# Optimization experiments

Measured on AMD Instinct MI355X. Metric: run time of the kernel, lower is better.

Reference implementation:

```python
import jax, jax.numpy as jnp
import numpy as np

B, D, K, H, E, Z = 64, 25000, 16, 128, 256, 32


def setup_inputs() -> dict:
    key = jax.random.key(0)
    ks = jax.random.split(key, 10)
    s = 0.02
    return {
        "x": jax.random.normal(ks[0], (B, D), jnp.float32),
        "mask": jax.random.randint(ks[1], (B, D), 0, 2, jnp.int32),
        "feat_emb": jax.random.normal(ks[2], (D, K), jnp.float32),          # feature_embedding [D,K]
        "feat_bias": jnp.zeros((D, 1), jnp.float32),                        # feature_bias [D,1]
        "W1": jax.random.normal(ks[3], (1 + K + 1, H), jnp.float32) * s,    # h_layer linear 1 (in,out)
        "b1": jnp.zeros((H,), jnp.float32),
        "W2": jax.random.normal(ks[4], (H, K), jnp.float32) * s,            # h_layer linear 2
        "b2": jnp.zeros((K,), jnp.float32),
        "We1": jax.random.normal(ks[5], (K, E), jnp.float32) * s,           # encoder_mlp linear 1
        "be1": jnp.zeros((E,), jnp.float32),
        "We2": jax.random.normal(ks[6], (E, 2 * Z), jnp.float32) * s,       # encoder_mlp linear 2
        "be2": jnp.zeros((2 * Z,), jnp.float32),
    }


def reference(x, mask, feat_emb, feat_bias, W1, b1, W2, b2, We1, be1, We2, be2):
    b, d = x.shape
    k = feat_emb.shape[1]
    # Build per-(sample, feature) input rows: [x_bd, F_d(K), bias_d] -> [B, D, 1+K+1]
    h_in = jnp.concatenate(
        [
            x[:, :, None],
            jnp.broadcast_to(feat_emb[None, :, :], (b, d, k)),
            jnp.broadcast_to(feat_bias[None, :, :], (b, d, 1)),
        ],
        axis=-1,
    )
    # Shared small MLP (h_layer), dropout is identity at rate 0.0
    h = jax.nn.relu(h_in @ W1 + b1)          # [B, D, H]
    h = jax.nn.relu(h @ W2 + b2)             # [B, D, K]
    # Masked sum pooling over features
    c = jnp.sum(h * mask.astype(h.dtype)[:, :, None], axis=1)  # [B, K]
    # encoder_mlp
    enc = jax.nn.relu(c @ We1 + be1) @ We2 + be2                # [B, 2Z]
    mu, logvar = jnp.split(enc, 2, axis=-1)
    return mu, logvar
```

## Files before the change

### kernel.cpp

```cpp
#include <hip/hip_runtime.h>
#include <hip/hip_bf16.h>

#define B 64
#define D 25000
#define K 16
#define H 128
#define E 256
#define Z 32
#define DTILE 20
#define NBLK (D / DTILE)
#define NREP 8
#define MSTR 68

#define REP_BYTES (NREP * B * K * 4)
#define HI_OFF    REP_BYTES

typedef __attribute__((ext_vector_type(8))) _Float16 half8;
typedef __attribute__((ext_vector_type(2))) _Float16 hv2;
typedef __attribute__((ext_vector_type(4))) float f32x4;

__global__ __launch_bounds__(256) void prep_kernel(
    const float* __restrict__ W2, float* __restrict__ rep, _Float16* __restrict__ hi)
{
    const int t = threadIdx.x;
    const int bid = blockIdx.x;
    if (bid < NREP) {
        for (int i = t; i < B * K; i += 256) rep[bid * B * K + i] = 0.f;
    } else {
        for (int i = t; i < H * K; i += 256) {
            int j = i & 7, n = (i >> 3) & 15, g = (i >> 7) & 3, s = i >> 9;
            int k = s * 32 + g * 8 + j;
            hi[i] = (_Float16)W2[k * K + n];
        }
    }
}

__global__ __launch_bounds__(256) void partial_main_kernel(
    const float* __restrict__ x, const int* __restrict__ mask,
    const float* __restrict__ feat_emb, const float* __restrict__ feat_bias,
    const float* __restrict__ W1, const float* __restrict__ b1,
    const float* __restrict__ b2, const _Float16* __restrict__ hi,
    float* __restrict__ rep)
{
    __shared__ __align__(16) _Float16 sGh[DTILE * H];
    __shared__ __align__(16) float sMf[DTILE * MSTR];

    const int t    = threadIdx.x;
    const int d0   = blockIdx.x * DTILE;
    const int lane = t & 63;
    const int wv   = t >> 6;
    const int g    = lane >> 4;
    const int n    = lane & 15;

    for (int i = t; i < DTILE * B; i += 256) {
        int bb = i / DTILE, dd = i - bb * DTILE;
        sMf[dd * MSTR + bb] = (float)mask[bb * D + d0 + dd];
    }
    for (int i = t; i < DTILE * H; i += 256) {
        int dd = i >> 7, h = i & (H - 1);
        int d = d0 + dd;
        float acc = fmaf(feat_bias[d], W1[17 * H + h], b1[h]);
        #pragma unroll
        for (int k = 0; k < K; ++k)
            acc = fmaf(feat_emb[d * K + k], W1[(1 + k) * H + h], acc);
        sGh[i] = (_Float16)acc;
    }

    const float* xrow = x + (size_t)(wv * 16 + n) * D + d0;
    hv2 xh[DTILE / 2];
    #pragma unroll
    for (int i = 0; i < DTILE / 4; ++i) {
        float4 xv = *(const float4*)(xrow + 4 * i);
        xh[2 * i]     = (hv2){(_Float16)xv.x, (_Float16)xv.y};
        xh[2 * i + 1] = (hv2){(_Float16)xv.z, (_Float16)xv.w};
    }

    half8 Bf[4];
    #pragma unroll
    for (int s = 0; s < 4; ++s)
        Bf[s] = *(const half8*)(hi + (((s * 4 + g) * 16 + n) << 3));
    hv2 w0h[4][4];
    #pragma unroll
    for (int s = 0; s < 4; ++s) {
        const float4* wp = (const float4*)&W1[s * 32 + g * 8];
        float4 a0 = wp[0], a1 = wp[1];
        w0h[s][0] = (hv2){(_Float16)a0.x, (_Float16)a0.y};
        w0h[s][1] = (hv2){(_Float16)a0.z, (_Float16)a0.w};
        w0h[s][2] = (hv2){(_Float16)a1.x, (_Float16)a1.y};
        w0h[s][3] = (hv2){(_Float16)a1.z, (_Float16)a1.w};
    }
    const float b2n = b2[n];
    const hv2 zeroh = {(_Float16)0.f, (_Float16)0.f};
    __syncthreads();

    f32x4 cacc = {0.f, 0.f, 0.f, 0.f};
    const int moff = wv * 16 + g * 4;
    const _Float16* gb0 = sGh + g * 8;

    #pragma unroll
    for (int i = 0; i < DTILE / 2; ++i) {
        const int dd0 = 2 * i, dd1 = 2 * i + 1;
        const hv2 xa = {xh[i].x, xh[i].x};
        const hv2 xb = {xh[i].y, xh[i].y};
        f32x4 c1a = {b2n, b2n, b2n, b2n};
        f32x4 c1b = {b2n, b2n, b2n, b2n};
        #pragma unroll
        for (int s = 0; s < 4; ++s) {
            union GA { half8 v; hv2 p[4]; };
            GA ga, gb, A0, A1;
            ga.v = *(const half8*)(gb0 + dd0 * H + s * 32);
            gb.v = *(const half8*)(gb0 + dd1 * H + s * 32);
            #pragma unroll
            for (int p = 0; p < 4; ++p) {
                hv2 h0 = __builtin_elementwise_fma(xa, w0h[s][p], ga.p[p]);
                hv2 h1 = __builtin_elementwise_fma(xb, w0h[s][p], gb.p[p]);
                A0.p[p] = __builtin_elementwise_max(h0, zeroh);
                A1.p[p] = __builtin_elementwise_max(h1, zeroh);
            }
            c1a = __builtin_amdgcn_mfma_f32_16x16x32_f16(A0.v, Bf[s], c1a, 0, 0, 0);
            c1b = __builtin_amdgcn_mfma_f32_16x16x32_f16(A1.v, Bf[s], c1b, 0, 0, 0);
        }
        const float4 mv0 = *(const float4*)&sMf[dd0 * MSTR + moff];
        const float4 mv1 = *(const float4*)&sMf[dd1 * MSTR + moff];
        cacc[0] = fmaf(mv0.x, fmaxf(c1a[0], 0.f), fmaf(mv1.x, fmaxf(c1b[0], 0.f), cacc[0]));
        cacc[1] = fmaf(mv0.y, fmaxf(c1a[1], 0.f), fmaf(mv1.y, fmaxf(c1b[1], 0.f), cacc[1]));
        cacc[2] = fmaf(mv0.z, fmaxf(c1a[2], 0.f), fmaf(mv1.z, fmaxf(c1b[2], 0.f), cacc[2]));
        cacc[3] = fmaf(mv0.w, fmaxf(c1a[3], 0.f), fmaf(mv1.w, fmaxf(c1b[3], 0.f), cacc[3]));
    }

    float* crep = rep + (size_t)(blockIdx.x & (NREP - 1)) * (B * K);
    #pragma unroll
    for (int r = 0; r < 4; ++r)
        atomicAdd(&crep[(moff + r) * K + n], cacc[r]);
}

__global__ __launch_bounds__(256) void partial_enc_kernel(
    const float* __restrict__ rep, const float* __restrict__ We1,
    const float* __restrict__ be1, const float* __restrict__ We2,
    const float* __restrict__ be2, float* __restrict__ out)
{
    const int b = blockIdx.x;
    const int t = threadIdx.x;
    __shared__ float sc[K];
    __shared__ float st1[E];
    __shared__ float red[256];

    {
        const int k = t & 15, grp = t >> 4;
        red[t] = (grp < NREP) ? rep[grp * (B * K) + b * K + k] : 0.f;
    }
    __syncthreads();
    if (t < K) {
        float s2 = 0.f;
        #pragma unroll
        for (int q = 0; q < 16; ++q) s2 += red[q * 16 + t];
        sc[t] = s2;
    }
    __syncthreads();

    {
        float acc = be1[t];
        #pragma unroll
        for (int k = 0; k < K; ++k)
            acc = fmaf(sc[k], We1[k * E + t], acc);
        st1[t] = fmaxf(acc, 0.f);
    }
    __syncthreads();

    const int j = t & 63, seg = t >> 6;
    float acc = 0.f;
    #pragma unroll 4
    for (int e = seg * 64; e < seg * 64 + 64; ++e)
        acc = fmaf(st1[e], We2[e * 64 + j], acc);
    red[t] = acc;
    __syncthreads();

    if (t < 64) {
        float v = red[j] + red[64 + j] + red[128 + j] + red[192 + j] + be2[j];
        if (j < Z) out[b * Z + j] = v;
        else       out[B * Z + b * Z + (j - Z)] = v;
    }
}

extern "C" void kernel_launch(void* const* d_in, const int* in_sizes, int n_in,
                              void* d_out, int out_size, void* d_ws, size_t ws_size,
                              hipStream_t stream) {
    const float* x         = (const float*)d_in[0];
    const int*   mask      = (const int*)  d_in[1];
    const float* feat_emb  = (const float*)d_in[2];
    const float* feat_bias = (const float*)d_in[3];
    const float* W1        = (const float*)d_in[4];
    const float* b1        = (const float*)d_in[5];
    const float* W2        = (const float*)d_in[6];
    const float* b2        = (const float*)d_in[7];
    const float* We1       = (const float*)d_in[8];
    const float* be1       = (const float*)d_in[9];
    const float* We2       = (const float*)d_in[10];
    const float* be2       = (const float*)d_in[11];

    float*     rep = (float*)d_ws;
    _Float16*  hi  = (_Float16*)((char*)d_ws + HI_OFF);

    prep_kernel<<<NREP + 1, 256, 0, stream>>>(W2, rep, hi);
    partial_main_kernel<<<NBLK, 256, 0, stream>>>(
        x, mask, feat_emb, feat_bias, W1, b1, b2, hi, rep);
    partial_enc_kernel<<<B, 256, 0, stream>>>(
        rep, We1, be1, We2, be2, (float*)d_out);
}
```

Measured before the change: 115.4 us.

## Replace atomic reduction with per-block slots and drop W2 prep kernel

Each main-kernel block now writes its partial pooled sums to its own workspace slot instead of atomically adding into 8 replicas. The encoder kernel then sums all per-block slots itself. The W2-to-fp16 conversion moves into the main kernel as strided global loads, which removes the separate prep launch and the zeroing pass. The change also register-double-buffers the LDS loads of the per-feature hidden term and adds an occupancy hint to launch_bounds. The trade is atomic contention for several MB of extra slot writes and a long serial reduction over 1250 slots spread across only 64 encoder blocks.

Result: slower. 196.7 us (+70.5%).

```diff
diff --git a/kernel.cpp b/kernel.cpp
--- a/kernel.cpp
+++ b/kernel.cpp
@@ -9,38 +9,18 @@
 #define Z 32
 #define DTILE 20
 #define NBLK (D / DTILE)
-#define NREP 8
 #define MSTR 68
-
-#define REP_BYTES (NREP * B * K * 4)
-#define HI_OFF    REP_BYTES
 
 typedef __attribute__((ext_vector_type(8))) _Float16 half8;
 typedef __attribute__((ext_vector_type(2))) _Float16 hv2;
 typedef __attribute__((ext_vector_type(4))) float f32x4;
 
-__global__ __launch_bounds__(256) void prep_kernel(
-    const float* __restrict__ W2, float* __restrict__ rep, _Float16* __restrict__ hi)
-{
-    const int t = threadIdx.x;
-    const int bid = blockIdx.x;
-    if (bid < NREP) {
-        for (int i = t; i < B * K; i += 256) rep[bid * B * K + i] = 0.f;
-    } else {
-        for (int i = t; i < H * K; i += 256) {
-            int j = i & 7, n = (i >> 3) & 15, g = (i >> 7) & 3, s = i >> 9;
-            int k = s * 32 + g * 8 + j;
-            hi[i] = (_Float16)W2[k * K + n];
-        }
-    }
-}
-
-__global__ __launch_bounds__(256) void partial_main_kernel(
+__global__ __launch_bounds__(256, 4) void partial_main_kernel(
     const float* __restrict__ x, const int* __restrict__ mask,
     const float* __restrict__ feat_emb, const float* __restrict__ feat_bias,
     const float* __restrict__ W1, const float* __restrict__ b1,
-    const float* __restrict__ b2, const _Float16* __restrict__ hi,
-    float* __restrict__ rep)
+    const float* __restrict__ W2, const float* __restrict__ b2,
+    float* __restrict__ slots)
 {
     __shared__ __align__(16) _Float16 sGh[DTILE * H];
     __shared__ __align__(16) float sMf[DTILE * MSTR];
@@ -75,10 +55,14 @@
         xh[2 * i + 1] = (hv2){(_Float16)xv.z, (_Float16)xv.w};
     }
 
-    half8 Bf[4];
+    union HB { half8 v; _Float16 e[8]; };
+    HB Bf[4];
     #pragma unroll
     for (int s = 0; s < 4; ++s)
-        Bf[s] = *(const half8*)(hi + (((s * 4 + g) * 16 + n) << 3));
+        #pragma unroll
+        for (int j = 0; j < 8; ++j)
+            Bf[s].e[j] = (_Float16)W2[(s * 32 + g * 8 + j) * K + n];
+
     hv2 w0h[4][4];
     #pragma unroll
     for (int s = 0; s < 4; ++s) {
@@ -97,45 +81,61 @@
     const int moff = wv * 16 + g * 4;
     const _Float16* gb0 = sGh + g * 8;
 
+    union GA { half8 v; hv2 p[4]; };
+    GA cur0[4], cur1[4];
+    #pragma unroll
+    for (int s = 0; s < 4; ++s) {
+        cur0[s].v = *(const half8*)(gb0 + 0 * H + s * 32);
+        cur1[s].v = *(const half8*)(gb0 + 1 * H + s * 32);
+    }
+
     #pragma unroll
     for (int i = 0; i < DTILE / 2; ++i) {
-        const int dd0 = 2 * i, dd1 = 2 * i + 1;
+        GA nxt0[4], nxt1[4];
+        if (i + 1 < DTILE / 2) {
+            #pragma unroll
+            for (int s = 0; s < 4; ++s) {
+                nxt0[s].v = *(const half8*)(gb0 + (2 * i + 2) * H + s * 32);
+                nxt1[s].v = *(const half8*)(gb0 + (2 * i + 3) * H + s * 32);
+            }
+        }
         const hv2 xa = {xh[i].x, xh[i].x};
         const hv2 xb = {xh[i].y, xh[i].y};
         f32x4 c1a = {b2n, b2n, b2n, b2n};
         f32x4 c1b = {b2n, b2n, b2n, b2n};
         #pragma unroll
         for (int s = 0; s < 4; ++s) {
-            union GA { half8 v; hv2 p[4]; };
-            GA ga, gb, A0, A1;
-            ga.v = *(const half8*)(gb0 + dd0 * H + s * 32);
-            gb.v = *(const half8*)(gb0 + dd1 * H + s * 32);
+            GA A0, A1;
             #pragma unroll
             for (int p = 0; p < 4; ++p) {
-                hv2 h0 = __builtin_elementwise_fma(xa, w0h[s][p], ga.p[p]);
-                hv2 h1 = __builtin_elementwise_fma(xb, w0h[s][p], gb.p[p]);
+                hv2 h0 = __builtin_elementwise_fma(xa, w0h[s][p], cur0[s].p[p]);
+                hv2 h1 = __builtin_elementwise_fma(xb, w0h[s][p], cur1[s].p[p]);
                 A0.p[p] = __builtin_elementwise_max(h0, zeroh);
                 A1.p[p] = __builtin_elementwise_max(h1, zeroh);
             }
-            c1a = __builtin_amdgcn_mfma_f32_16x16x32_f16(A0.v, Bf[s], c1a, 0, 0, 0);
-            c1b = __builtin_amdgcn_mfma_f32_16x16x32_f16(A1.v, Bf[s], c1b, 0, 0, 0);
+            c1a = __builtin_amdgcn_mfma_f32_16x16x32_f16(A0.v, Bf[s].v, c1a, 0, 0, 0);
+            c1b = __builtin_amdgcn_mfma_f32_16x16x32_f16(A1.v, Bf[s].v, c1b, 0, 0, 0);
         }
-        const float4 mv0 = *(const float4*)&sMf[dd0 * MSTR + moff];
-        const float4 mv1 = *(const float4*)&sMf[dd1 * MSTR + moff];
+        const float4 mv0 = *(const float4*)&sMf[(2 * i) * MSTR + moff];
+        const float4 mv1 = *(const float4*)&sMf[(2 * i + 1) * MSTR + moff];
         cacc[0] = fmaf(mv0.x, fmaxf(c1a[0], 0.f), fmaf(mv1.x, fmaxf(c1b[0], 0.f), cacc[0]));
         cacc[1] = fmaf(mv0.y, fmaxf(c1a[1], 0.f), fmaf(mv1.y, fmaxf(c1b[1], 0.f), cacc[1]));
         cacc[2] = fmaf(mv0.z, fmaxf(c1a[2], 0.f), fmaf(mv1.z, fmaxf(c1b[2], 0.f), cacc[2]));
         cacc[3] = fmaf(mv0.w, fmaxf(c1a[3], 0.f), fmaf(mv1.w, fmaxf(c1b[3], 0.f), cacc[3]));
-    }
-
-    float* crep = rep + (size_t)(blockIdx.x & (NREP - 1)) * (B * K);
+        if (i + 1 < DTILE / 2) {
+            #pragma unroll
+            for (int s = 0; s < 4; ++s) { cur0[s] = nxt0[s]; cur1[s] = nxt1[s]; }
+        }
+    }
+
+    float* slot = slots + (size_t)blockIdx.x * (B * K);
     #pragma unroll
     for (int r = 0; r < 4; ++r)
-        atomicAdd(&crep[(moff + r) * K + n], cacc[r]);
+        slot[(moff + r) * K + n] = cacc[r];
 }
 
 __global__ __launch_bounds__(256) void partial_enc_kernel(
-    const float* __restrict__ rep, const float* __restrict__ We1,
+    const float* __restrict__ slots, const float* __restrict__ We1,
     const float* __restrict__ be1, const float* __restrict__ We2,
     const float* __restrict__ be2, float* __restrict__ out)
 {
@@ -147,7 +147,10 @@
 
     {
         const int k = t & 15, grp = t >> 4;
-        red[t] = (grp < NREP) ? rep[grp * (B * K) + b * K + k] : 0.f;
+        float a = 0.f;
+        for (int blk = grp; blk < NBLK; blk += 16)
+            a += slots[(size_t)blk * (B * K) + b * K + k];
+        red[t] = a;
     }
     __syncthreads();
     if (t < K) {
@@ -198,12 +201,10 @@
     const float* We2       = (const float*)d_in[10];
     const float* be2       = (const float*)d_in[11];
 
-    float*     rep = (float*)d_ws;
-    _Float16*  hi  = (_Float16*)((char*)d_ws + HI_OFF);
-
-    prep_kernel<<<NREP + 1, 256, 0, stream>>>(W2, rep, hi);
+    float* slots = (float*)d_ws;
+
     partial_main_kernel<<<NBLK, 256, 0, stream>>>(
-        x, mask, feat_emb, feat_bias, W1, b1, b2, hi, rep);
+        x, mask, feat_emb, feat_bias, W1, b1, W2, b2, slots);
     partial_enc_kernel<<<B, 256, 0, stream>>>(
-        rep, We1, be1, We2, be2, (float*)d_out);
+        slots, We1, be1, We2, be2, (float*)d_out);
 }
```

## Halve feature tile per block and vectorize feature-embedding loads

Applied to the files above, without the earlier changes.

Drops DTILE from 20 to 10, which doubles the block count to 2500 so more waves are resident. The x loads move from float4 to float2 to match the smaller tile. The per-feature hidden precompute now reads feat_emb as float4 vectors and splits the dot product into two accumulators to shorten the dependency chain. The cost is twice as many blocks, more atomics into the replicated partial sums, and more redundant loading of per-block weights.

Result: no change. 113.4 us (-1.7%).

```diff
diff --git a/kernel.cpp b/kernel.cpp
--- a/kernel.cpp
+++ b/kernel.cpp
@@ -7,7 +7,7 @@
 #define H 128
 #define E 256
 #define Z 32
-#define DTILE 20
+#define DTILE 10
 #define NBLK (D / DTILE)
 #define NREP 8
 #define MSTR 68
@@ -59,20 +59,35 @@
     for (int i = t; i < DTILE * H; i += 256) {
         int dd = i >> 7, h = i & (H - 1);
         int d = d0 + dd;
-        float acc = fmaf(feat_bias[d], W1[17 * H + h], b1[h]);
-        #pragma unroll
-        for (int k = 0; k < K; ++k)
-            acc = fmaf(feat_emb[d * K + k], W1[(1 + k) * H + h], acc);
-        sGh[i] = (_Float16)acc;
+        const float4* fe = (const float4*)&feat_emb[d * K];
+        float4 f0 = fe[0], f1 = fe[1], f2 = fe[2], f3 = fe[3];
+        float accA = fmaf(feat_bias[d], W1[17 * H + h], b1[h]);
+        float accB = 0.f;
+        accA = fmaf(f0.x, W1[(1 + 0) * H + h], accA);
+        accB = fmaf(f0.y, W1[(1 + 1) * H + h], accB);
+        accA = fmaf(f0.z, W1[(1 + 2) * H + h], accA);
+        accB = fmaf(f0.w, W1[(1 + 3) * H + h], accB);
+        accA = fmaf(f1.x, W1[(1 + 4) * H + h], accA);
+        accB = fmaf(f1.y, W1[(1 + 5) * H + h], accB);
+        accA = fmaf(f1.z, W1[(1 + 6) * H + h], accA);
+        accB = fmaf(f1.w, W1[(1 + 7) * H + h], accB);
+        accA = fmaf(f2.x, W1[(1 + 8) * H + h], accA);
+        accB = fmaf(f2.y, W1[(1 + 9) * H + h], accB);
+        accA = fmaf(f2.z, W1[(1 + 10) * H + h], accA);
+        accB = fmaf(f2.w, W1[(1 + 11) * H + h], accB);
+        accA = fmaf(f3.x, W1[(1 + 12) * H + h], accA);
+        accB = fmaf(f3.y, W1[(1 + 13) * H + h], accB);
+        accA = fmaf(f3.z, W1[(1 + 14) * H + h], accA);
+        accB = fmaf(f3.w, W1[(1 + 15) * H + h], accB);
+        sGh[i] = (_Float16)(accA + accB);
     }
 
     const float* xrow = x + (size_t)(wv * 16 + n) * D + d0;
     hv2 xh[DTILE / 2];
     #pragma unroll
-    for (int i = 0; i < DTILE / 4; ++i) {
-        float4 xv = *(const float4*)(xrow + 4 * i);
-        xh[2 * i]     = (hv2){(_Float16)xv.x, (_Float16)xv.y};
-        xh[2 * i + 1] = (hv2){(_Float16)xv.z, (_Float16)xv.w};
+    for (int i = 0; i < DTILE / 2; ++i) {
+        float2 xv = *(const float2*)(xrow + 2 * i);
+        xh[i] = (hv2){(_Float16)xv.x, (_Float16)xv.y};
     }
 
     half8 Bf[4];
```

## Compute per-feature first-layer projection with MFMA and halve feature tile

Applied to the files above, without the earlier changes.

Replaces the scalar per-thread FMA loop that projects feat_emb and feat_bias through W1 (plus b1) with a single 16x16x32 f16 MFMA per wave per column chunk. W1 and b1 are prepacked into an f16 fragment layout by an extra prep block. DTILE drops from 20 to 10 so one MFMA M-tile covers the tile, doubling the block count. This cuts VALU work in the prologue but adds f16 rounding of the embedding inputs and more blocks and atomics.

Measured after the change: 113.2 us. About the same (-1.9%).

```diff
diff --git a/kernel.cpp b/kernel.cpp
--- a/kernel.cpp
+++ b/kernel.cpp
@@ -7,30 +7,46 @@
 #define H 128
 #define E 256
 #define Z 32
-#define DTILE 20
+#define DTILE 10
 #define NBLK (D / DTILE)
 #define NREP 8
 #define MSTR 68
 
 #define REP_BYTES (NREP * B * K * 4)
 #define HI_OFF    REP_BYTES
+#define W1F_OFF   (HI_OFF + H * K * 2)
 
 typedef __attribute__((ext_vector_type(8))) _Float16 half8;
 typedef __attribute__((ext_vector_type(2))) _Float16 hv2;
 typedef __attribute__((ext_vector_type(4))) float f32x4;
 
 __global__ __launch_bounds__(256) void prep_kernel(
-    const float* __restrict__ W2, float* __restrict__ rep, _Float16* __restrict__ hi)
+    const float* __restrict__ W1, const float* __restrict__ b1,
+    const float* __restrict__ W2, float* __restrict__ rep,
+    _Float16* __restrict__ hiW2, _Float16* __restrict__ w1f)
 {
     const int t = threadIdx.x;
     const int bid = blockIdx.x;
     if (bid < NREP) {
         for (int i = t; i < B * K; i += 256) rep[bid * B * K + i] = 0.f;
-    } else {
+    } else if (bid == NREP) {
         for (int i = t; i < H * K; i += 256) {
             int j = i & 7, n = (i >> 3) & 15, g = (i >> 7) & 3, s = i >> 9;
             int k = s * 32 + g * 8 + j;
-            hi[i] = (_Float16)W2[k * K + n];
+            hiW2[i] = (_Float16)W2[k * K + n];
+        }
+    } else {
+        for (int i = t; i < 8 * 64 * 8; i += 256) {
+            int j = i & 7, lane = (i >> 3) & 63, c = i >> 9;
+            int g = lane >> 4, n = lane & 15;
+            int k = g * 8 + j;
+            int h = c * 16 + n;
+            float v;
+            if (k < 16)       v = W1[(1 + k) * H + h];
+            else if (k == 16) v = W1[17 * H + h];
+            else if (k == 17) v = b1[h];
+            else              v = 0.f;
+            w1f[i] = (_Float16)v;
         }
     }
 }
@@ -38,8 +54,8 @@
 __global__ __launch_bounds__(256) void partial_main_kernel(
     const float* __restrict__ x, const int* __restrict__ mask,
     const float* __restrict__ feat_emb, const float* __restrict__ feat_bias,
-    const float* __restrict__ W1, const float* __restrict__ b1,
-    const float* __restrict__ b2, const _Float16* __restrict__ hi,
+    const float* __restrict__ W1, const float* __restrict__ b2,
+    const _Float16* __restrict__ hiW2, const _Float16* __restrict__ w1f,
     float* __restrict__ rep)
 {
     __shared__ __align__(16) _Float16 sGh[DTILE * H];
@@ -56,29 +72,53 @@
         int bb = i / DTILE, dd = i - bb * DTILE;
         sMf[dd * MSTR + bb] = (float)mask[bb * D + d0 + dd];
     }
-    for (int i = t; i < DTILE * H; i += 256) {
-        int dd = i >> 7, h = i & (H - 1);
-        int d = d0 + dd;
-        float acc = fmaf(feat_bias[d], W1[17 * H + h], b1[h]);
-        #pragma unroll
-        for (int k = 0; k < K; ++k)
-            acc = fmaf(feat_emb[d * K + k], W1[(1 + k) * H + h], acc);
-        sGh[i] = (_Float16)acc;
+
+    {
+        const int m  = n;
+        const int dA = min(d0 + m, D - 1);
+        union AF { half8 v; _Float16 e[8]; } af;
+        if (g < 2) {
+            const float4* fe = (const float4*)&feat_emb[(size_t)dA * K + g * 8];
+            float4 u0 = fe[0], u1 = fe[1];
+            af.e[0] = (_Float16)u0.x; af.e[1] = (_Float16)u0.y;
+            af.e[2] = (_Float16)u0.z; af.e[3] = (_Float16)u0.w;
+            af.e[4] = (_Float16)u1.x; af.e[5] = (_Float16)u1.y;
+            af.e[6] = (_Float16)u1.z; af.e[7] = (_Float16)u1.w;
+        } else if (g == 2) {
+            af.e[0] = (_Float16)feat_bias[dA];
+            af.e[1] = (_Float16)1.f;
+            #pragma unroll
+            for (int j = 2; j < 8; ++j) af.e[j] = (_Float16)0.f;
+        } else {
+            #pragma unroll
+            for (int j = 0; j < 8; ++j) af.e[j] = (_Float16)0.f;
+        }
+        #pragma unroll
+        for (int cc = 0; cc < 2; ++cc) {
+            const int c = wv * 2 + cc;
+            half8 bf = *(const half8*)(w1f + (((c << 6) + lane) << 3));
+            f32x4 C = {0.f, 0.f, 0.f, 0.f};
+            C = __builtin_amdgcn_mfma_f32_16x16x32_f16(af.v, bf, C, 0, 0, 0);
+            #pragma unroll
+            for (int r = 0; r < 4; ++r) {
+                const int m2 = g * 4 + r;
+                if (m2 < DTILE) sGh[m2 * H + c * 16 + n] = (_Float16)C[r];
+            }
+        }
     }
 
     const float* xrow = x + (size_t)(wv * 16 + n) * D + d0;
     hv2 xh[DTILE / 2];
     #pragma unroll
-    for (int i = 0; i < DTILE / 4; ++i) {
-        float4 xv = *(const float4*)(xrow + 4 * i);
-        xh[2 * i]     = (hv2){(_Float16)xv.x, (_Float16)xv.y};
-        xh[2 * i + 1] = (hv2){(_Float16)xv.z, (_Float16)xv.w};
+    for (int i = 0; i < DTILE / 2; ++i) {
+        float2 xv = *(const float2*)(xrow + 2 * i);
+        xh[i] = (hv2){(_Float16)xv.x, (_Float16)xv.y};
     }
 
     half8 Bf[4];
     #pragma unroll
     for (int s = 0; s < 4; ++s)
-        Bf[s] = *(const half8*)(hi + (((s * 4 + g) * 16 + n) << 3));
+        Bf[s] = *(const half8*)(hiW2 + (((s * 4 + g) * 16 + n) << 3));
     hv2 w0h[4][4];
     #pragma unroll
     for (int s = 0; s < 4; ++s) {
@@ -198,12 +238,13 @@
     const float* We2       = (const float*)d_in[10];
     const float* be2       = (const float*)d_in[11];
 
-    float*     rep = (float*)d_ws;
-    _Float16*  hi  = (_Float16*)((char*)d_ws + HI_OFF);
-
-    prep_kernel<<<NREP + 1, 256, 0, stream>>>(W2, rep, hi);
+    float*     rep  = (float*)d_ws;
+    _Float16*  hiW2 = (_Float16*)((char*)d_ws + HI_OFF);
+    _Float16*  w1f  = (_Float16*)((char*)d_ws + W1F_OFF);
+
+    prep_kernel<<<NREP + 2, 256, 0, stream>>>(W1, b1, W2, rep, hiW2, w1f);
     partial_main_kernel<<<NBLK, 256, 0, stream>>>(
-        x, mask, feat_emb, feat_bias, W1, b1, b2, hi, rep);
+        x, mask, feat_emb, feat_bias, W1, b2, hiW2, w1f, rep);
     partial_enc_kernel<<<B, 256, 0, stream>>>(
         rep, We1, be1, We2, be2, (float*)d_out);
 }
```
